# Kernel optimization log

Measured on AMD Instinct MI355X. Metric: run time of the kernel, lower is better.

Reference implementation:

```python
import jax, jax.numpy as jnp
import numpy as np

EMBED = 1024
DFF = 4096


def _layernorm(x, g, b, eps=1e-5):
    mu = jnp.mean(x, axis=-1, keepdims=True)
    var = jnp.var(x, axis=-1, keepdims=True)
    return (x - mu) * jax.lax.rsqrt(var + eps) * g + b


def setup_inputs() -> dict:
    key = jax.random.key(0)
    ks = jax.random.split(key, 14)
    s = 1.0 / np.sqrt(EMBED)
    sf = 1.0 / np.sqrt(DFF)
    d = {
        "src": jax.random.normal(ks[0], (4, 2048, EMBED), dtype=jnp.float32),
        "Wq": jax.random.uniform(ks[1], (EMBED, EMBED), jnp.float32, -s, s),
        "bq": jnp.zeros((EMBED,), jnp.float32),
        "Wk": jax.random.uniform(ks[2], (EMBED, EMBED), jnp.float32, -s, s),
        "bk": jnp.zeros((EMBED,), jnp.float32),
        "Wv": jax.random.uniform(ks[3], (EMBED, EMBED), jnp.float32, -s, s),
        "bv": jnp.zeros((EMBED,), jnp.float32),
        "Wo": jax.random.uniform(ks[4], (EMBED, EMBED), jnp.float32, -s, s),
        "bo": jnp.zeros((EMBED,), jnp.float32),
        "W1": jax.random.uniform(ks[5], (EMBED, DFF), jnp.float32, -s, s),
        "b1": jnp.zeros((DFF,), jnp.float32),
        "W2": jax.random.uniform(ks[6], (DFF, EMBED), jnp.float32, -sf, sf),
        "b2": jnp.zeros((EMBED,), jnp.float32),
        "g1": jnp.ones((EMBED,), jnp.float32),
        "be1": jnp.zeros((EMBED,), jnp.float32),
        "g2": jnp.ones((EMBED,), jnp.float32),
        "be2": jnp.zeros((EMBED,), jnp.float32),
    }
    return d


def reference(src, Wq, bq, Wk, bk, Wv, bv, Wo, bo, W1, b1, W2, b2, g1, be1, g2, be2):
    # Q/K/V projections: [b, s, d]
    Q = src @ Wq + bq
    K = src @ Wk + bk
    V = src @ Wv + bv
    # Single-head, UNSCALED attention (faithful to source: no 1/sqrt(d), num_heads unused)
    scores = jnp.einsum("bqd,bkd->bqk", Q, K)  # [b, s, s]
    weights = jax.nn.softmax(scores, axis=-1)
    attn = jnp.einsum("bqk,bkd->bqd", weights, V)
    attn = attn @ Wo + bo
    x = _layernorm(src + attn, g1, be1)
    ff = jax.nn.relu(x @ W1 + b1) @ W2 + b2
    return _layernorm(x + ff, g2, be2)
```

## Files before the change

kernel.cpp:

```cpp
#include <hip/hip_runtime.h>
#include <stdint.h>

typedef unsigned short u16;
typedef _Float16 v8h __attribute__((ext_vector_type(8)));
typedef float v4f __attribute__((ext_vector_type(4)));

static __device__ __forceinline__ float h2f(u16 u) {
    union { u16 s; _Float16 h; } v; v.s = u; return (float)v.h;
}
static __device__ __forceinline__ u16 f2h(float f) {
    union { u16 s; _Float16 h; } v; v.h = (_Float16)f; return v.s;
}

static __device__ __forceinline__ void gload_lds16(const u16* g, const u16* l) {
    __builtin_amdgcn_global_load_lds(
        (const __attribute__((address_space(1))) uint32_t*)(uintptr_t)g,
        (__attribute__((address_space(3))) uint32_t*)(uintptr_t)l,
        16, 0, 0);
}

__global__ __launch_bounds__(256) void cvt_f16(const float* __restrict__ in,
                                               u16* __restrict__ out, int n8) {
    const int i = blockIdx.x * 256 + threadIdx.x;
    if (i >= n8) return;
    const float4 a = ((const float4*)in)[2 * i];
    const float4 b = ((const float4*)in)[2 * i + 1];
    u16 o[8] = {f2h(a.x), f2h(a.y), f2h(a.z), f2h(a.w),
                f2h(b.x), f2h(b.y), f2h(b.z), f2h(b.w)};
    *(uint4*)(out + (size_t)i * 8) = *(const uint4*)o;
}

__global__ __launch_bounds__(256) void transpose_all(
    const float* __restrict__ Wq, const float* __restrict__ Wk,
    const float* __restrict__ Wv, const float* __restrict__ Wo,
    const float* __restrict__ W1, const float* __restrict__ W2,
    u16* __restrict__ WqkvT, u16* __restrict__ WoT,
    u16* __restrict__ W1T, u16* __restrict__ W2T)
{
    int t = blockIdx.x;
    const float* in; u16* out; long ldi, ldo; int xt;
    if (t < 1024)      {            in = Wq; out = WqkvT;               ldi = 1024; ldo = 1024; xt = 32; }
    else if (t < 2048) { t -= 1024; in = Wk; out = WqkvT + 1024*1024;   ldi = 1024; ldo = 1024; xt = 32; }
    else if (t < 3072) { t -= 2048; in = Wv; out = WqkvT + 2*1024*1024; ldi = 1024; ldo = 1024; xt = 32; }
    else if (t < 4096) { t -= 3072; in = Wo; out = WoT;                 ldi = 1024; ldo = 1024; xt = 32; }
    else if (t < 8192) { t -= 4096; in = W1; out = W1T;                 ldi = 4096; ldo = 1024; xt = 128; }
    else               { t -= 8192; in = W2; out = W2T;                 ldi = 1024; ldo = 4096; xt = 32; }
    const int c0 = (t % xt) * 32, r0 = (t / xt) * 32;
    __shared__ float tile[32][33];
    for (int i = threadIdx.y; i < 32; i += 8)
        tile[i][threadIdx.x] = in[(long)(r0 + i) * ldi + c0 + threadIdx.x];
    __syncthreads();
    for (int i = threadIdx.y; i < 32; i += 8)
        out[(long)(c0 + i) * ldo + r0 + threadIdx.x] = f2h(tile[threadIdx.x][i]);
}

template<int OMODE, int BIAS, bool RELU, int NX, int NY, int NZ>
__global__ __launch_bounds__(512) void gemm256(
    const u16* __restrict__ A, long lda, long Asb,
    const u16* __restrict__ B, long ldb, long Bsb,
    void* __restrict__ Cv, long ldc, long Csb, u16* __restrict__ C1,
    const float* __restrict__ bias, const float* __restrict__ bias2,
    const float* __restrict__ bias3, int K)
{
    constexpr int NWG = NX * NY * NZ;
    static_assert(NWG % 8 == 0, "XCD swizzle needs nwg % 8 == 0");
    alignas(16) __shared__ u16 As[4 * 8192];
    alignas(16) __shared__ u16 Bs[4 * 8192];

    const int tid = threadIdx.x;
    const int lane = tid & 63, wave = tid >> 6;
    const int l16 = lane & 15, quad = lane >> 4;
    const int wm = wave >> 2;
    const int wn = wave & 3;

    const int lin = blockIdx.x;
    const int tl = (lin & 7) * (NWG / 8) + (lin >> 3);
    const int xe = tl % NX;
    const int ye = (tl / NX) % NY;
    const int zb = tl / (NX * NY);
    const long m0 = (long)ye * 256;
    const long n0 = (long)xe * 256;

    const u16* Aop = A + (long)zb * Asb;
    const u16* Bop = B + (long)zb * Bsb;

    const int srow = tid >> 2;
    const int sq = (tid & 3) ^ ((tid >> 3) & 3);
    const long gaofs0 = (m0 + srow) * lda + sq * 8;
    const long gaofs1 = gaofs0 + 128 * lda;
    const long gbofs0 = (n0 + srow) * ldb + sq * 8;
    const long gbofs1 = gbofs0 + 128 * ldb;
    const int wv512n = wave * 512;

    const int swzE = (quad ^ ((l16 >> 1) & 3)) * 8;
    const int aRow = (wm * 128 + l16) * 32 + swzE;
    const int bRow = (wn * 64 + l16) * 32 + swzE;

    v4f acc[8][4];
#pragma unroll
    for (int i = 0; i < 8; ++i)
#pragma unroll
        for (int j = 0; j < 4; ++j)
            acc[i][j] = (v4f){0.f, 0.f, 0.f, 0.f};
    v8h af[4];
    v8h bfr[2][4];

#define STAGE_A(RIDX, KP) do { \
        u16* lb_ = As + (RIDX) * 8192 + wv512n; \
        gload_lds16(Aop + gaofs0 + (KP), lb_); \
        gload_lds16(Aop + gaofs1 + (KP), lb_ + 4096); } while (0)
#define STAGE_B(RIDX, KP) do { \
        u16* lb_ = Bs + (RIDX) * 8192 + wv512n; \
        gload_lds16(Bop + gbofs0 + (KP), lb_); \
        gload_lds16(Bop + gbofs1 + (KP), lb_ + 4096); } while (0)

#define MF4(CH, I, BC) \
    acc[(CH)*4+(I)][0] = __builtin_amdgcn_mfma_f32_16x16x32_f16(af[I], bfr[BC][0], acc[(CH)*4+(I)][0], 0, 0, 0); \
    acc[(CH)*4+(I)][1] = __builtin_amdgcn_mfma_f32_16x16x32_f16(af[I], bfr[BC][1], acc[(CH)*4+(I)][1], 0, 0, 0); \
    acc[(CH)*4+(I)][2] = __builtin_amdgcn_mfma_f32_16x16x32_f16(af[I], bfr[BC][2], acc[(CH)*4+(I)][2], 0, 0, 0); \
    acc[(CH)*4+(I)][3] = __builtin_amdgcn_mfma_f32_16x16x32_f16(af[I], bfr[BC][3], acc[(CH)*4+(I)][3], 0, 0, 0);

#define PHASE(CH, BC, NRD, NCH, BLN, BN, ODD, STG) { \
        STG; \
        __builtin_amdgcn_s_setprio(1); \
        MF4(CH, 0, BC) \
        MF4(CH, 1, BC) \
        { const u16* Ar_ = As + (NRD) * 8192 + aRow + (NCH) * 2048; \
          af[0] = *(const v8h*)(Ar_); \
          af[1] = *(const v8h*)(Ar_ + 512); \
          if (BLN) { const u16* Br_ = Bs + (NRD) * 8192 + bRow; \
            bfr[BN][0] = *(const v8h*)(Br_); \
            bfr[BN][1] = *(const v8h*)(Br_ + 512); \
            bfr[BN][2] = *(const v8h*)(Br_ + 1024); \
            bfr[BN][3] = *(const v8h*)(Br_ + 1536); } } \
        MF4(CH, 2, BC) \
        { const u16* Ar_ = As + (NRD) * 8192 + aRow + (NCH) * 2048; \
          af[2] = *(const v8h*)(Ar_ + 1024); } \
        MF4(CH, 3, BC) \
        { const u16* Ar_ = As + (NRD) * 8192 + aRow + (NCH) * 2048; \
          af[3] = *(const v8h*)(Ar_ + 1536); } \
        __builtin_amdgcn_s_setprio(0); \
        if (ODD) asm volatile("s_waitcnt vmcnt(6)" ::: "memory"); \
        __builtin_amdgcn_s_barrier(); \
    }

    STAGE_A(0, 0);  STAGE_B(0, 0);
    STAGE_A(1, 32); STAGE_B(1, 32);
    STAGE_A(2, 64); STAGE_B(2, 64);
    asm volatile("s_waitcnt vmcnt(8)" ::: "memory");
    __builtin_amdgcn_s_barrier();

#pragma unroll
    for (int i = 0; i < 4; ++i) af[i] = *(const v8h*)&As[aRow + i * 512];
#pragma unroll
    for (int j = 0; j < 4; ++j) bfr[0][j] = *(const v8h*)&Bs[bRow + j * 512];

    const int NT = K >> 7;
#pragma unroll 1
    for (int t = 0; t < NT; ++t) {
        const long kb = (long)t * 128;
        const long kp1 = kb + 96;
        long kp2  = kb + 128; if (kp2  >= K) kp2  = 0;
        long kp2b = kb + 160; if (kp2b >= K) kp2b = 0;
        long kp3  = kb + 192; if (kp3  >= K) kp3  = 0;

        PHASE(0, 0,  0,  1,  0, 0, 1, STAGE_A(3, kp1))
        PHASE(1, 0,  1,  0,  1, 1, 0, STAGE_B(3, kp1))
        PHASE(0, 1,  1,  1,  0, 0, 1, STAGE_A(0, kp2))
        PHASE(1, 1,  2,  0,  1, 0, 0, STAGE_B(0, kp2))
        PHASE(0, 0,  2,  1,  0, 0, 1, STAGE_A(1, kp2b))
        PHASE(1, 0,  3,  0,  1, 1, 0, STAGE_B(1, kp2b))
        PHASE(0, 1,  3,  1,  0, 0, 1, STAGE_A(2, kp3))
        PHASE(1, 1,  0,  0,  1, 0, 0, STAGE_B(2, kp3))
    }

    asm volatile("s_waitcnt vmcnt(0) lgkmcnt(0)" ::: "memory");
    __builtin_amdgcn_s_barrier();

#undef PHASE
#undef MF4
#undef STAGE_A
#undef STAGE_B

    float bv[4];
#pragma unroll
    for (int j = 0; j < 4; ++j) {
        const long col = n0 + wn * 64 + j * 16 + l16;
        if (BIAS == 0) bv[j] = 0.f;
        else if (BIAS == 1) bv[j] = bias[col];
        else {
            const int sel = (int)(col >> 10);
            const float* bp = sel == 0 ? bias : (sel == 1 ? bias2 : bias3);
            bv[j] = bp[col & 1023];
        }
    }

    if (OMODE == 3 && n0 >= 2048) {
        const long bb = m0 >> 11, mb = m0 & 2047;
        u16* C = C1 + bb * Csb;
#pragma unroll
        for (int j = 0; j < 4; ++j) {
            const long col = n0 - 2048 + wn * 64 + j * 16 + l16;
            u16* pc = C + col * 2048 + mb + wm * 128 + quad * 4;
#pragma unroll
            for (int i = 0; i < 8; ++i) {
                u16 o[4];
#pragma unroll
                for (int r = 0; r < 4; ++r) {
                    float val = acc[i][j][r] + bv[j];
                    if (RELU) val = fmaxf(val, 0.f);
                    o[r] = f2h(val);
                }
                *(uint2*)(pc + i * 16) = *(const uint2*)o;
            }
        }
    } else {
        const long cb = (OMODE == 3 ? 0 : (long)zb * Csb)
                      + (m0 + wm * 128 + quad * 4) * ldc + (n0 + wn * 64 + l16);
        u16* p0 = (u16*)Cv + cb;
#pragma unroll
        for (int i = 0; i < 8; ++i)
#pragma unroll
            for (int r = 0; r < 4; ++r) {
                u16* prow = p0 + (long)(i * 16 + r) * ldc;
#pragma unroll
                for (int j = 0; j < 4; ++j) {
                    float val = acc[i][j][r] + bv[j];
                    if (RELU) val = fmaxf(val, 0.f);
                    prow[j * 16] = f2h(val);
                }
            }
    }
}

template<int OMODE, int BIAS, bool RELU, int NX, int NY, int NZ>
__global__ __launch_bounds__(512) void gemm256n(
    const u16* __restrict__ A, long lda, long Asb,
    const u16* __restrict__ B, long ldb, long Bsb,
    void* __restrict__ Cv, long ldc, long Csb, u16* __restrict__ C1,
    const float* __restrict__ bias, const float* __restrict__ bias2,
    const float* __restrict__ bias3, int K)
{
    constexpr int NWG = NX * NY * NZ;
    static_assert(NWG % 8 == 0, "XCD swizzle needs nwg % 8 == 0");
    alignas(16) __shared__ u16 As[4 * 8192];
    alignas(16) __shared__ u16 Bs[4 * 4096];

    const int tid = threadIdx.x;
    const int lane = tid & 63, wave = tid >> 6;
    const int l16 = lane & 15, quad = lane >> 4;
    const int wm = wave >> 2;
    const int wn = wave & 3;

    const int lin = blockIdx.x;
    const int tl = (lin & 7) * (NWG / 8) + (lin >> 3);
    const int xe = tl % NX;
    const int ye = (tl / NX) % NY;
    const int zb = tl / (NX * NY);
    const long m0 = (long)ye * 256;
    const long n0 = (long)xe * 128;

    const u16* Aop = A + (long)zb * Asb;
    const u16* Bop = B + (long)zb * Bsb;

    const int srow = tid >> 2;
    const int sq = (tid & 3) ^ ((tid >> 3) & 3);
    const long gaofs0 = (m0 + srow) * lda + sq * 8;
    const long gaofs1 = gaofs0 + 128 * lda;
    const long gbofs0 = (n0 + srow) * ldb + sq * 8;
    const int wv512n = wave * 512;

    const int swzE = (quad ^ ((l16 >> 1) & 3)) * 8;
    const int aRow = (wm * 128 + l16) * 32 + swzE;
    const int bRow = (wn * 32 + l16) * 32 + swzE;

    v4f acc[8][2];
#pragma unroll
    for (int i = 0; i < 8; ++i)
#pragma unroll
        for (int j = 0; j < 2; ++j)
            acc[i][j] = (v4f){0.f, 0.f, 0.f, 0.f};
    v8h bf[2];

#define STAGE_A(RIDX, KP) do { \
        u16* lb_ = As + (RIDX) * 8192 + wv512n; \
        gload_lds16(Aop + gaofs0 + (KP), lb_); \
        gload_lds16(Aop + gaofs1 + (KP), lb_ + 4096); } while (0)
#define STAGE_B(RIDX, KP) do { \
        gload_lds16(Bop + gbofs0 + (KP), Bs + (RIDX) * 4096 + wv512n); } while (0)

#define MF2(CH, I) \
    acc[(CH) * 4 + (I)][0] = __builtin_amdgcn_mfma_f32_16x16x32_f16(af[I], bf[0], acc[(CH) * 4 + (I)][0], 0, 0, 0); \
    acc[(CH) * 4 + (I)][1] = __builtin_amdgcn_mfma_f32_16x16x32_f16(af[I], bf[1], acc[(CH) * 4 + (I)][1], 0, 0, 0);

#define PHASE(BUF, KH, CH, EVENW, ...) { \
        if (EVENW) asm volatile("s_waitcnt vmcnt(5)" ::: "memory"); \
        const u16* Ar_ = As + ((BUF) * 2 + (KH)) * 8192 + aRow + (CH) * 2048; \
        v8h af[4]; \
        af[0] = *(const v8h*)(Ar_); \
        af[1] = *(const v8h*)(Ar_ + 512); \
        af[2] = *(const v8h*)(Ar_ + 1024); \
        af[3] = *(const v8h*)(Ar_ + 1536); \
        if ((CH) == 0) { \
            const u16* Br_ = Bs + ((BUF) * 2 + (KH)) * 4096 + bRow; \
            bf[0] = *(const v8h*)(Br_); \
            bf[1] = *(const v8h*)(Br_ + 512); \
        } \
        __VA_ARGS__; \
        __builtin_amdgcn_s_barrier(); \
        asm volatile("s_waitcnt lgkmcnt(0)" ::: "memory"); \
        __builtin_amdgcn_s_setprio(1); \
        MF2(CH, 0) \
        MF2(CH, 1) \
        MF2(CH, 2) \
        MF2(CH, 3) \
        __builtin_amdgcn_s_setprio(0); \
        __builtin_amdgcn_s_barrier(); \
    }

    STAGE_A(0, 0);  STAGE_B(0, 0);
    STAGE_A(1, 32); STAGE_B(1, 32);
    STAGE_A(2, 64); STAGE_B(2, 64);
    asm volatile("s_waitcnt vmcnt(6)" ::: "memory");
    __builtin_amdgcn_s_barrier();

    const int NT = K >> 7;
#pragma unroll 1
    for (int t = 0; t < NT; ++t) {
        const long kb = (long)t * 128;
        const long kp1 = kb + 96;
        long kp2  = kb + 128; if (kp2  >= K) kp2  = 0;
        long kp2b = kb + 160; if (kp2b >= K) kp2b = 0;
        long kp3  = kb + 192; if (kp3  >= K) kp3  = 0;

        PHASE(0, 0, 0, false, STAGE_A(3, kp1))
        PHASE(0, 0, 1, true,  STAGE_B(3, kp1))
        PHASE(0, 1, 0, false, STAGE_A(0, kp2))
        PHASE(0, 1, 1, true,  STAGE_B(0, kp2))
        PHASE(1, 0, 0, false, STAGE_A(1, kp2b))
        PHASE(1, 0, 1, true,  STAGE_B(1, kp2b))
        PHASE(1, 1, 0, false, STAGE_A(2, kp3))
        PHASE(1, 1, 1, true,  STAGE_B(2, kp3))
    }

#undef PHASE
#undef MF2
#undef STAGE_A
#undef STAGE_B

    float bv[2];
#pragma unroll
    for (int j = 0; j < 2; ++j) {
        const long col = n0 + wn * 32 + j * 16 + l16;
        if (BIAS == 0) bv[j] = 0.f;
        else if (BIAS == 1) bv[j] = bias[col];
        else {
            const int sel = (int)(col >> 10);
            const float* bp = sel == 0 ? bias : (sel == 1 ? bias2 : bias3);
            bv[j] = bp[col & 1023];
        }
    }

    if (OMODE == 3 && n0 >= 2048) {
        const long bb = m0 >> 11, mb = m0 & 2047;
        u16* C = C1 + bb * Csb;
#pragma unroll
        for (int j = 0; j < 2; ++j) {
            const long col = n0 - 2048 + wn * 32 + j * 16 + l16;
            u16* pc = C + col * 2048 + mb + wm * 128 + quad * 4;
#pragma unroll
            for (int i = 0; i < 8; ++i) {
                u16 o[4];
#pragma unroll
                for (int r = 0; r < 4; ++r) {
                    float val = acc[i][j][r] + bv[j];
                    if (RELU) val = fmaxf(val, 0.f);
                    o[r] = f2h(val);
                }
                *(uint2*)(pc + i * 16) = *(const uint2*)o;
            }
        }
    } else {
        const long cb = (OMODE == 3 ? 0 : (long)zb * Csb)
                      + (m0 + wm * 128 + quad * 4) * ldc + (n0 + wn * 32 + l16);
        u16* p0 = (u16*)Cv + cb;
#pragma unroll
        for (int i = 0; i < 8; ++i)
#pragma unroll
            for (int r = 0; r < 4; ++r) {
                u16* prow = p0 + (long)(i * 16 + r) * ldc;
#pragma unroll
                for (int j = 0; j < 2; ++j) {
                    float val = acc[i][j][r] + bv[j];
                    if (RELU) val = fmaxf(val, 0.f);
                    prow[j * 16] = f2h(val);
                }
            }
    }
}

__global__ __launch_bounds__(256) void softmax_rows(u16* __restrict__ S) {
    const long row = blockIdx.x;
    u16* p = S + row * 2048;
    const int t = threadIdx.x;
    float v[8];
    float mx = -1e30f;
#pragma unroll
    for (int i = 0; i < 8; ++i) { v[i] = h2f(p[t + i * 256]); mx = fmaxf(mx, v[i]); }
    __shared__ float red[256];
    red[t] = mx; __syncthreads();
    for (int off = 128; off > 0; off >>= 1) {
        if (t < off) red[t] = fmaxf(red[t], red[t + off]);
        __syncthreads();
    }
    mx = red[0]; __syncthreads();
    float sum = 0.f;
#pragma unroll
    for (int i = 0; i < 8; ++i) { v[i] = __expf(v[i] - mx); sum += v[i]; }
    red[t] = sum; __syncthreads();
    for (int off = 128; off > 0; off >>= 1) {
        if (t < off) red[t] += red[t + off];
        __syncthreads();
    }
    const float inv = 1.f / red[0];
#pragma unroll
    for (int i = 0; i < 8; ++i) p[t + i * 256] = f2h(v[i] * inv);
}

__global__ __launch_bounds__(256) void ln_one(
    const float* __restrict__ a, const u16* __restrict__ bb,
    const float* __restrict__ g, const float* __restrict__ be,
    u16* __restrict__ out16)
{
    const long base = (long)blockIdx.x * 1024;
    const int t = threadIdx.x;
    float v[4]; float s = 0.f, ss = 0.f;
#pragma unroll
    for (int i = 0; i < 4; ++i) {
        const int c = t + i * 256;
        const float x = a[base + c] + h2f(bb[base + c]);
        v[i] = x; s += x; ss += x * x;
    }
    __shared__ float rs[256], rss[256];
    rs[t] = s; rss[t] = ss; __syncthreads();
    for (int off = 128; off > 0; off >>= 1) {
        if (t < off) { rs[t] += rs[t + off]; rss[t] += rss[t + off]; }
        __syncthreads();
    }
    const float mean = rs[0] * (1.f / 1024.f);
    const float var = rss[0] * (1.f / 1024.f) - mean * mean;
    const float rstd = rsqrtf(var + 1e-5f);
#pragma unroll
    for (int i = 0; i < 4; ++i) {
        const int c = t + i * 256;
        out16[base + c] = f2h((v[i] - mean) * rstd * g[c] + be[c]);
    }
}

__global__ __launch_bounds__(256) void ln_two(
    const u16* __restrict__ a, const u16* __restrict__ bb,
    const float* __restrict__ g, const float* __restrict__ be,
    float* __restrict__ out)
{
    const long base = (long)blockIdx.x * 1024;
    const int t = threadIdx.x;
    float v[4]; float s = 0.f, ss = 0.f;
#pragma unroll
    for (int i = 0; i < 4; ++i) {
        const int c = t + i * 256;
        const float x = h2f(a[base + c]) + h2f(bb[base + c]);
        v[i] = x; s += x; ss += x * x;
    }
    __shared__ float rs[256], rss[256];
    rs[t] = s; rss[t] = ss; __syncthreads();
    for (int off = 128; off > 0; off >>= 1) {
        if (t < off) { rs[t] += rs[t + off]; rss[t] += rss[t + off]; }
        __syncthreads();
    }
    const float mean = rs[0] * (1.f / 1024.f);
    const float var = rss[0] * (1.f / 1024.f) - mean * mean;
    const float rstd = rsqrtf(var + 1e-5f);
#pragma unroll
    for (int i = 0; i < 4; ++i) {
        const int c = t + i * 256;
        out[base + c] = (v[i] - mean) * rstd * g[c] + be[c];
    }
}

extern "C" void kernel_launch(void* const* d_in, const int* in_sizes, int n_in,
                              void* d_out, int out_size, void* d_ws, size_t ws_size,
                              hipStream_t stream) {
    (void)in_sizes; (void)n_in; (void)out_size; (void)ws_size;
    constexpr long S = 2048, E = 1024, F = 4096, M = 8192;

    const float* src = (const float*)d_in[0];
    const float* Wq  = (const float*)d_in[1];
    const float* bq  = (const float*)d_in[2];
    const float* Wk  = (const float*)d_in[3];
    const float* bk  = (const float*)d_in[4];
    const float* Wv  = (const float*)d_in[5];
    const float* bv  = (const float*)d_in[6];
    const float* Wo  = (const float*)d_in[7];
    const float* bo  = (const float*)d_in[8];
    const float* W1  = (const float*)d_in[9];
    const float* b1  = (const float*)d_in[10];
    const float* W2  = (const float*)d_in[11];
    const float* b2  = (const float*)d_in[12];
    const float* g1  = (const float*)d_in[13];
    const float* be1 = (const float*)d_in[14];
    const float* g2  = (const float*)d_in[15];
    const float* be2 = (const float*)d_in[16];

    char* ws = (char*)d_ws;
    size_t off = 0;
    auto take = [&](size_t bytes) {
        char* p = ws + off;
        off += (bytes + 255) & ~(size_t)255;
        return p;
    };
    const size_t MB16 = 16777216;
    u16*   srcH  = (u16*)take(MB16);
    u16*   WqkvT = (u16*)take(3 * E * E * 2);
    u16*   WoT   = (u16*)take(E * E * 2);
    u16*   W1T   = (u16*)take(F * E * 2);
    u16*   W2T   = (u16*)take(E * F * 2);
    char*  B0    = take(2 * MB16);
    char*  B1    = take(MB16);
    char*  B2    = take(4ull * S * S * 4);
    char*  B3    = take(MB16);
    char*  B4    = take(MB16);

    u16*   QK    = (u16*)B0;
    u16*   VT    = (u16*)B1;
    u16*   Sh    = (u16*)B2;
    u16*   hf    = (u16*)B2;
    u16*   attn  = (u16*)B3;
    u16*   xh    = (u16*)B3;
    u16*   attnO = (u16*)B4;
    u16*   ffO   = (u16*)B4;

    dim3 blk(256), blk5(512), tb(32, 8);

    cvt_f16<<<dim3(M * E / 8 / 256), blk, 0, stream>>>(src, srcH, M * E / 8);

    transpose_all<<<dim3(12288), tb, 0, stream>>>(Wq, Wk, Wv, Wo, W1, W2,
                                                  WqkvT, WoT, W1T, W2T);

    gemm256n<3, 3, false, 24, 32, 1><<<dim3(24 * 32), blk5, 0, stream>>>(
        srcH, E, 0, WqkvT, E, 0, QK, 2 * E, E * S, VT, bq, bk, bv, E);

    gemm256<0, 0, false, 8, 8, 4><<<dim3(8 * 8 * 4), blk5, 0, stream>>>(
        QK, 2 * E, S * 2 * E, QK + E, 2 * E, S * 2 * E,
        Sh, S, S * S, nullptr, nullptr, nullptr, nullptr, E);

    softmax_rows<<<dim3(M), blk, 0, stream>>>(Sh);

    gemm256n<0, 0, false, 8, 8, 4><<<dim3(8 * 8 * 4), blk5, 0, stream>>>(
        Sh, S, S * S, VT, S, E * S,
        attn, E, S * E, nullptr, nullptr, nullptr, nullptr, S);

    gemm256n<0, 1, false, 8, 32, 1><<<dim3(8 * 32), blk5, 0, stream>>>(
        attn, E, 0, WoT, E, 0, attnO, E, 0, nullptr, bo, nullptr, nullptr, E);

    ln_one<<<dim3(M), blk, 0, stream>>>(src, attnO, g1, be1, xh);

    gemm256<0, 1, true, 16, 32, 1><<<dim3(16 * 32), blk5, 0, stream>>>(
        xh, E, 0, W1T, E, 0, hf, F, 0, nullptr, b1, nullptr, nullptr, E);

    gemm256n<0, 1, false, 8, 32, 1><<<dim3(8 * 32), blk5, 0, stream>>>(
        hf, F, 0, W2T, F, 0, ffO, E, 0, nullptr, b2, nullptr, nullptr, F);

    ln_two<<<dim3(M), blk, 0, stream>>>(xh, ffO, g2, be2, (float*)d_out);
}
```

Baseline: 504.5 us.

## Reshape gemm256n wave tiling to 4x2 and halve B staging buffers

```diff
diff --git a/kernel.cpp b/kernel.cpp
--- a/kernel.cpp
+++ b/kernel.cpp
@@ -234,7 +234,7 @@
 }
 
 template<int OMODE, int BIAS, bool RELU, int NX, int NY, int NZ>
-__global__ __launch_bounds__(512) void gemm256n(
+__global__ __launch_bounds__(512, 4) void gemm256n(
     const u16* __restrict__ A, long lda, long Asb,
     const u16* __restrict__ B, long ldb, long Bsb,
     void* __restrict__ Cv, long ldc, long Csb, u16* __restrict__ C1,
@@ -244,13 +244,13 @@
     constexpr int NWG = NX * NY * NZ;
     static_assert(NWG % 8 == 0, "XCD swizzle needs nwg % 8 == 0");
     alignas(16) __shared__ u16 As[4 * 8192];
-    alignas(16) __shared__ u16 Bs[4 * 4096];
+    alignas(16) __shared__ u16 Bs[2 * 4096];
 
     const int tid = threadIdx.x;
     const int lane = tid & 63, wave = tid >> 6;
     const int l16 = lane & 15, quad = lane >> 4;
-    const int wm = wave >> 2;
-    const int wn = wave & 3;
+    const int wm = wave >> 1;
+    const int wn = wave & 1;
 
     const int lin = blockIdx.x;
     const int tl = (lin & 7) * (NWG / 8) + (lin >> 3);
@@ -271,87 +271,87 @@
     const int wv512n = wave * 512;
 
     const int swzE = (quad ^ ((l16 >> 1) & 3)) * 8;
-    const int aRow = (wm * 128 + l16) * 32 + swzE;
-    const int bRow = (wn * 32 + l16) * 32 + swzE;
-
-    v4f acc[8][2];
-#pragma unroll
-    for (int i = 0; i < 8; ++i)
-#pragma unroll
-        for (int j = 0; j < 2; ++j)
+    const int aRow = (wm * 64 + l16) * 32 + swzE;
+    const int bRow = (wn * 64 + l16) * 32 + swzE;
+
+    v4f acc[4][4];
+#pragma unroll
+    for (int i = 0; i < 4; ++i)
+#pragma unroll
+        for (int j = 0; j < 4; ++j)
             acc[i][j] = (v4f){0.f, 0.f, 0.f, 0.f};
-    v8h bf[2];
+    v8h bf[4];
 
 #define STAGE_A(RIDX, KP) do { \
         u16* lb_ = As + (RIDX) * 8192 + wv512n; \
         gload_lds16(Aop + gaofs0 + (KP), lb_); \
         gload_lds16(Aop + gaofs1 + (KP), lb_ + 4096); } while (0)
-#define STAGE_B(RIDX, KP) do { \
-        gload_lds16(Bop + gbofs0 + (KP), Bs + (RIDX) * 4096 + wv512n); } while (0)
-
-#define MF2(CH, I) \
-    acc[(CH) * 4 + (I)][0] = __builtin_amdgcn_mfma_f32_16x16x32_f16(af[I], bf[0], acc[(CH) * 4 + (I)][0], 0, 0, 0); \
-    acc[(CH) * 4 + (I)][1] = __builtin_amdgcn_mfma_f32_16x16x32_f16(af[I], bf[1], acc[(CH) * 4 + (I)][1], 0, 0, 0);
-
-#define PHASE(BUF, KH, CH, EVENW, ...) { \
-        if (EVENW) asm volatile("s_waitcnt vmcnt(5)" ::: "memory"); \
-        const u16* Ar_ = As + ((BUF) * 2 + (KH)) * 8192 + aRow + (CH) * 2048; \
-        v8h af[4]; \
-        af[0] = *(const v8h*)(Ar_); \
-        af[1] = *(const v8h*)(Ar_ + 512); \
-        af[2] = *(const v8h*)(Ar_ + 1024); \
-        af[3] = *(const v8h*)(Ar_ + 1536); \
+#define STAGE_B(SLOT, KP) do { \
+        gload_lds16(Bop + gbofs0 + (KP), Bs + (SLOT) * 4096 + wv512n); } while (0)
+
+#define PHASE(BUF, KH, CH, EVENW, STG) { \
+        if (EVENW) asm volatile("s_waitcnt vmcnt(2)" ::: "memory"); \
+        const u16* Ar_ = As + ((BUF) * 2 + (KH)) * 8192 + aRow + (CH) * 1024; \
+        v8h af0 = *(const v8h*)(Ar_); \
+        v8h af1 = *(const v8h*)(Ar_ + 512); \
         if ((CH) == 0) { \
-            const u16* Br_ = Bs + ((BUF) * 2 + (KH)) * 4096 + bRow; \
+            const u16* Br_ = Bs + (KH) * 4096 + bRow; \
             bf[0] = *(const v8h*)(Br_); \
             bf[1] = *(const v8h*)(Br_ + 512); \
+            bf[2] = *(const v8h*)(Br_ + 1024); \
+            bf[3] = *(const v8h*)(Br_ + 1536); \
         } \
-        __VA_ARGS__; \
+        STG; \
         __builtin_amdgcn_s_barrier(); \
         asm volatile("s_waitcnt lgkmcnt(0)" ::: "memory"); \
         __builtin_amdgcn_s_setprio(1); \
-        MF2(CH, 0) \
-        MF2(CH, 1) \
-        MF2(CH, 2) \
-        MF2(CH, 3) \
+        acc[(CH)*2+0][0] = __builtin_amdgcn_mfma_f32_16x16x32_f16(af0, bf[0], acc[(CH)*2+0][0], 0, 0, 0); \
+        acc[(CH)*2+0][1] = __builtin_amdgcn_mfma_f32_16x16x32_f16(af0, bf[1], acc[(CH)*2+0][1], 0, 0, 0); \
+        acc[(CH)*2+0][2] = __builtin_amdgcn_mfma_f32_16x16x32_f16(af0, bf[2], acc[(CH)*2+0][2], 0, 0, 0); \
+        acc[(CH)*2+0][3] = __builtin_amdgcn_mfma_f32_16x16x32_f16(af0, bf[3], acc[(CH)*2+0][3], 0, 0, 0); \
+        acc[(CH)*2+1][0] = __builtin_amdgcn_mfma_f32_16x16x32_f16(af1, bf[0], acc[(CH)*2+1][0], 0, 0, 0); \
+        acc[(CH)*2+1][1] = __builtin_amdgcn_mfma_f32_16x16x32_f16(af1, bf[1], acc[(CH)*2+1][1], 0, 0, 0); \
+        acc[(CH)*2+1][2] = __builtin_amdgcn_mfma_f32_16x16x32_f16(af1, bf[2], acc[(CH)*2+1][2], 0, 0, 0); \
+        acc[(CH)*2+1][3] = __builtin_amdgcn_mfma_f32_16x16x32_f16(af1, bf[3], acc[(CH)*2+1][3], 0, 0, 0); \
         __builtin_amdgcn_s_setprio(0); \
         __builtin_amdgcn_s_barrier(); \
     }
 
     STAGE_A(0, 0);  STAGE_B(0, 0);
     STAGE_A(1, 32); STAGE_B(1, 32);
-    STAGE_A(2, 64); STAGE_B(2, 64);
-    asm volatile("s_waitcnt vmcnt(6)" ::: "memory");
+    STAGE_A(2, 64);
+    asm volatile("s_waitcnt vmcnt(5)" ::: "memory");
     __builtin_amdgcn_s_barrier();
 
     const int NT = K >> 7;
 #pragma unroll 1
     for (int t = 0; t < NT; ++t) {
         const long kb = (long)t * 128;
-        const long kp1 = kb + 96;
         long kp2  = kb + 128; if (kp2  >= K) kp2  = 0;
         long kp2b = kb + 160; if (kp2b >= K) kp2b = 0;
         long kp3  = kb + 192; if (kp3  >= K) kp3  = 0;
 
-        PHASE(0, 0, 0, false, STAGE_A(3, kp1))
-        PHASE(0, 0, 1, true,  STAGE_B(3, kp1))
+        PHASE(0, 0, 0, false, STAGE_A(3, kb + 96))
+        PHASE(0, 0, 1, true,  STAGE_B(0, kb + 64))
         PHASE(0, 1, 0, false, STAGE_A(0, kp2))
-        PHASE(0, 1, 1, true,  STAGE_B(0, kp2))
+        PHASE(0, 1, 1, true,  STAGE_B(1, kb + 96))
         PHASE(1, 0, 0, false, STAGE_A(1, kp2b))
-        PHASE(1, 0, 1, true,  STAGE_B(1, kp2b))
+        PHASE(1, 0, 1, true,  STAGE_B(0, kp2))
         PHASE(1, 1, 0, false, STAGE_A(2, kp3))
-        PHASE(1, 1, 1, true,  STAGE_B(2, kp3))
-    }
+        PHASE(1, 1, 1, true,  STAGE_B(1, kp2b))
+    }
+
+    asm volatile("s_waitcnt vmcnt(0) lgkmcnt(0)" ::: "memory");
+    __builtin_amdgcn_s_barrier();
 
 #undef PHASE
-#undef MF2
 #undef STAGE_A
 #undef STAGE_B
 
-    float bv[2];
-#pragma unroll
-    for (int j = 0; j < 2; ++j) {
-        const long col = n0 + wn * 32 + j * 16 + l16;
+    float bv[4];
+#pragma unroll
+    for (int j = 0; j < 4; ++j) {
+        const long col = n0 + wn * 64 + j * 16 + l16;
         if (BIAS == 0) bv[j] = 0.f;
         else if (BIAS == 1) bv[j] = bias[col];
         else {
@@ -365,11 +365,11 @@
         const long bb = m0 >> 11, mb = m0 & 2047;
         u16* C = C1 + bb * Csb;
 #pragma unroll
-        for (int j = 0; j < 2; ++j) {
-            const long col = n0 - 2048 + wn * 32 + j * 16 + l16;
-            u16* pc = C + col * 2048 + mb + wm * 128 + quad * 4;
-#pragma unroll
-            for (int i = 0; i < 8; ++i) {
+        for (int j = 0; j < 4; ++j) {
+            const long col = n0 - 2048 + wn * 64 + j * 16 + l16;
+            u16* pc = C + col * 2048 + mb + wm * 64 + quad * 4;
+#pragma unroll
+            for (int i = 0; i < 4; ++i) {
                 u16 o[4];
 #pragma unroll
                 for (int r = 0; r < 4; ++r) {
@@ -382,15 +382,15 @@
         }
     } else {
         const long cb = (OMODE == 3 ? 0 : (long)zb * Csb)
-                      + (m0 + wm * 128 + quad * 4) * ldc + (n0 + wn * 32 + l16);
+                      + (m0 + wm * 64 + quad * 4) * ldc + (n0 + wn * 64 + l16);
         u16* p0 = (u16*)Cv + cb;
 #pragma unroll
-        for (int i = 0; i < 8; ++i)
+        for (int i = 0; i < 4; ++i)
 #pragma unroll
             for (int r = 0; r < 4; ++r) {
                 u16* prow = p0 + (long)(i * 16 + r) * ldc;
 #pragma unroll
-                for (int j = 0; j < 2; ++j) {
+                for (int j = 0; j < 4; ++j) {
                     float val = acc[i][j][r] + bv[j];
                     if (RELU) val = fmaxf(val, 0.f);
                     prow[j * 16] = f2h(val);
```

Result: no change. 499.2 us (-1.1%).
